# Kernel tuning notes

Measured on AMD Instinct MI355X. Metric: run time of the kernel, lower is better.

## Reference

```python
import jax, jax.numpy as jnp
import numpy as np

B, S, D = 4, 2048, 1024

def setup_inputs() -> dict:
    key = jax.random.key(0)
    k0, k1, k2, k3, k4, k5 = jax.random.split(key, 6)
    scale = 1.0 / np.sqrt(D)
    return {
        "input_seq_embs": jax.random.normal(k0, (B, S, D), dtype=jnp.float32),
        "W_Q": jax.random.normal(k1, (D, D), dtype=jnp.float32) * scale,
        "W_K": jax.random.normal(k2, (D, D), dtype=jnp.float32) * scale,
        "W_V": jax.random.normal(k3, (D, D), dtype=jnp.float32) * scale,
        "W_O": jax.random.normal(k4, (D, D), dtype=jnp.float32) * scale,
        "b_O": jax.random.normal(k5, (D,), dtype=jnp.float32) * 0.01,
    }

def reference(input_seq_embs, W_Q, W_K, W_V, W_O, b_O):
    # torch nn.Linear: y = x @ W.T
    Q = jnp.einsum('bsd,ed->bse', input_seq_embs, W_Q)
    K = jnp.einsum('bsd,ed->bse', input_seq_embs, W_K)
    V = jnp.einsum('bsd,ed->bse', input_seq_embs, W_V)
    # NOTE: no 1/sqrt(d) scaling in the original module
    A = jnp.einsum('bqd,bkd->bqk', Q, K)  # [B,S,S]
    # log(tril(ones)) == 0 on/below diagonal, -inf above
    causal = jnp.tril(jnp.ones((S, S), dtype=bool))
    A = jnp.where(causal[None, :, :], A, -jnp.inf)
    A = jax.nn.softmax(A, axis=-1)
    # dropout layers are identity in eval mode
    out = jnp.einsum('bqk,bkd->bqd', A, V)
    out = jnp.einsum('bsd,ed->bse', out, W_O) + b_O
    return out
```

## Files before the change

### kernel.cpp

```cpp
#include <hip/hip_runtime.h>
#include <cstdint>

typedef _Float16 f16x8 __attribute__((ext_vector_type(8)));
typedef _Float16 f16x4 __attribute__((ext_vector_type(4)));
typedef float    f32x4 __attribute__((ext_vector_type(4)));

#define AS1 __attribute__((address_space(1)))
#define AS3 __attribute__((address_space(3)))

__device__ __forceinline__ void load16_lds(const void* g, void* l) {
  __builtin_amdgcn_global_load_lds((AS1 void*)g, (AS3 void*)l, 16, 0, 0);
}

#define GEMM_PROLOGUE(Ab, lda, Bb, ldb)                                   \
  __shared__ _Float16 lA[128 * 32];                                       \
  __shared__ _Float16 lB[128 * 32];                                       \
  int tid = threadIdx.x;                                                  \
  int r0 = tid >> 2;                                                      \
  int c0 = (tid & 3) * 8;                                                 \
  const _Float16* ga0 = Ab + (long long)r0 * lda + c0;                    \
  const _Float16* ga1 = Ab + (long long)(r0 + 64) * lda + c0;             \
  const _Float16* gb0 = Bb + (long long)r0 * ldb + c0;                    \
  const _Float16* gb1 = Bb + (long long)(r0 + 64) * ldb + c0;             \
  _Float16* la0 = lA + tid * 8;                                           \
  _Float16* la1 = lA + 2048 + tid * 8;                                    \
  _Float16* lb0 = lB + tid * 8;                                           \
  _Float16* lb1 = lB + 2048 + tid * 8;                                    \
  f32x4 acc[4][4] = {};                                                   \
  int lane = tid & 63;                                                    \
  int wv = tid >> 6;                                                      \
  int wm = (wv & 1) * 64, wn = (wv >> 1) * 64;                            \
  int l16 = lane & 15, quad = lane >> 4;                                  \
  const _Float16* raBase = lA + (wm + l16) * 32 + quad * 8;               \
  const _Float16* rbBase = lB + (wn + l16) * 32 + quad * 8;

#define GEMM_KLOOP(lda, ldb, KLEN, SWAP)                                  \
  for (int kb = 0; kb < (KLEN); kb += 32) {                               \
    __syncthreads();                                                      \
    load16_lds(ga0, la0);                                                 \
    load16_lds(ga1, la1);                                                 \
    load16_lds(gb0, lb0);                                                 \
    load16_lds(gb1, lb1);                                                 \
    ga0 += 32; ga1 += 32; gb0 += 32; gb1 += 32;                           \
    __syncthreads();                                                      \
    f16x8 af[4], bfr[4];                                                  \
    _Pragma("unroll")                                                     \
    for (int i = 0; i < 4; i++) af[i] = *(const f16x8*)(raBase + i * 512);\
    _Pragma("unroll")                                                     \
    for (int j = 0; j < 4; j++) bfr[j] = *(const f16x8*)(rbBase + j * 512);\
    _Pragma("unroll")                                                     \
    for (int i = 0; i < 4; i++)                                           \
      _Pragma("unroll")                                                   \
      for (int j = 0; j < 4; j++)                                         \
        acc[i][j] = (SWAP)                                                \
          ? __builtin_amdgcn_mfma_f32_16x16x32_f16(bfr[j], af[i], acc[i][j], 0, 0, 0) \
          : __builtin_amdgcn_mfma_f32_16x16x32_f16(af[i], bfr[j], acc[i][j], 0, 0, 0);\
  }

__global__ __launch_bounds__(256) void cvt_all(
    const float* __restrict__ x, const float* __restrict__ wq,
    const float* __restrict__ wk, const float* __restrict__ wv,
    const float* __restrict__ wo,
    _Float16* __restrict__ xh, _Float16* __restrict__ wcat,
    _Float16* __restrict__ woh) {
  long long g = (long long)blockIdx.x * 256 + threadIdx.x;
  const float* in; _Float16* out; long long idx;
  if (g < 2097152)      { in = x;  out = xh;             idx = g; }
  else if (g < 2359296) { in = wq; out = wcat;           idx = g - 2097152; }
  else if (g < 2621440) { in = wk; out = wcat + 1048576; idx = g - 2359296; }
  else if (g < 2883584) { in = wv; out = wcat + 2097152; idx = g - 2621440; }
  else                  { in = wo; out = woh;            idx = g - 2883584; }
  float4 v = ((const float4*)in)[idx];
  f16x4 o;
  o[0] = (_Float16)v.x; o[1] = (_Float16)v.y; o[2] = (_Float16)v.z; o[3] = (_Float16)v.w;
  ((f16x4*)out)[idx] = o;
}

__global__ __launch_bounds__(256) void qk_gemm(
    const _Float16* __restrict__ A, const _Float16* __restrict__ B,
    _Float16* __restrict__ Qh, _Float16* __restrict__ Kh) {
  int bx = blockIdx.x, by = blockIdx.y;
  const _Float16* Ab = A + (long long)by * 128 * 1024;
  const _Float16* Bb = B + (long long)bx * 128 * 1024;
  GEMM_PROLOGUE(Ab, 1024, Bb, 1024)
  GEMM_KLOOP(1024, 1024, 1024, true)

  _Float16* C = (bx < 8) ? Qh : Kh;
  int m0 = by * 128 + wm + l16;
  int n0 = (bx & 7) * 128 + wn + quad * 4;
  #pragma unroll
  for (int i = 0; i < 4; i++)
    #pragma unroll
    for (int j = 0; j < 4; j++) {
      f16x4 pk;
      #pragma unroll
      for (int r = 0; r < 4; r++) pk[r] = (_Float16)acc[i][j][r];
      *(f16x4*)(C + (long long)(m0 + i * 16) * 1024 + (n0 + j * 16)) = pk;
    }
}

__global__ __launch_bounds__(256) void v_gemm(
    const _Float16* __restrict__ A, const _Float16* __restrict__ B,
    _Float16* __restrict__ Vt) {
  int bx = blockIdx.x, by = blockIdx.y;
  const _Float16* Ab = A + (long long)by * 128 * 1024;
  const _Float16* Bb = B + (long long)bx * 128 * 1024;
  GEMM_PROLOGUE(Ab, 1024, Bb, 1024)
  GEMM_KLOOP(1024, 1024, 1024, false)

  int m0 = by * 128 + wm + quad * 4;
  int d0 = bx * 128 + wn + l16;
  #pragma unroll
  for (int i = 0; i < 4; i++) {
    long long mm = m0 + i * 16;
    long long b = mm >> 11;
    long long s = mm & 2047;
    #pragma unroll
    for (int j = 0; j < 4; j++) {
      f16x4 pk;
      #pragma unroll
      for (int r = 0; r < 4; r++) pk[r] = (_Float16)acc[i][j][r];
      *(f16x4*)(Vt + (b << 21) + (long long)(d0 + j * 16) * 2048 + s) = pk;
    }
  }
}

__global__ __launch_bounds__(256) void scores_gemm(
    const _Float16* __restrict__ Qh, const _Float16* __restrict__ Kh,
    _Float16* __restrict__ S, float2* __restrict__ stats) {
  int bx = blockIdx.x, by = blockIdx.y, bz = blockIdx.z;
  if (bx > by) return;
  const _Float16* Ab = Qh + (long long)bz * 2097152 + (long long)by * 128 * 1024;
  const _Float16* Bb = Kh + (long long)bz * 2097152 + (long long)bx * 128 * 1024;
  __shared__ float redM[128];
  __shared__ float redL[128];
  GEMM_PROLOGUE(Ab, 1024, Bb, 1024)
  GEMM_KLOOP(1024, 1024, 1024, true)

  bool diag = (bx == by);
  int rloc = wm + l16;
  int cloc = wn + quad * 4;

  float mloc[4];
  #pragma unroll
  for (int i = 0; i < 4; i++) {
    float mx = -3.0e38f;
    #pragma unroll
    for (int j = 0; j < 4; j++)
      #pragma unroll
      for (int r = 0; r < 4; r++) {
        bool ok = !diag || (cloc + j * 16 + r <= rloc + i * 16);
        mx = ok ? fmaxf(mx, acc[i][j][r]) : mx;
      }
    mx = fmaxf(mx, __shfl_xor(mx, 16));
    mx = fmaxf(mx, __shfl_xor(mx, 32));
    mloc[i] = mx;
  }
  __syncthreads();
  if (wn && quad == 0) {
    #pragma unroll
    for (int i = 0; i < 4; i++) redM[rloc + i * 16] = mloc[i];
  }
  __syncthreads();
  if (!wn) {
    #pragma unroll
    for (int i = 0; i < 4; i++) mloc[i] = fmaxf(mloc[i], redM[rloc + i * 16]);
  }
  __syncthreads();
  if (!wn && quad == 0) {
    #pragma unroll
    for (int i = 0; i < 4; i++) redM[rloc + i * 16] = mloc[i];
  }
  __syncthreads();
  float mfin[4];
  #pragma unroll
  for (int i = 0; i < 4; i++) mfin[i] = redM[rloc + i * 16];

  float lloc[4];
  #pragma unroll
  for (int i = 0; i < 4; i++) {
    float sum = 0.f;
    #pragma unroll
    for (int j = 0; j < 4; j++)
      #pragma unroll
      for (int r = 0; r < 4; r++) {
        bool ok = !diag || (cloc + j * 16 + r <= rloc + i * 16);
        float e = __expf(acc[i][j][r] - mfin[i]);
        sum += ok ? e : 0.f;
      }
    sum += __shfl_xor(sum, 16);
    sum += __shfl_xor(sum, 32);
    lloc[i] = sum;
  }
  if (wn && quad == 0) {
    #pragma unroll
    for (int i = 0; i < 4; i++) redL[rloc + i * 16] = lloc[i];
  }
  __syncthreads();
  if (!wn && quad == 0) {
    #pragma unroll
    for (int i = 0; i < 4; i++) {
      int rl = rloc + i * 16;
      float lt = lloc[i] + redL[rl];
      stats[((long long)bz * 2048 + by * 128 + rl) * 16 + bx] =
          make_float2(mfin[i], lt);
    }
  }

  _Float16* Sb = S + (long long)bz * 4194304;
  int gm = by * 128 + rloc;
  int gn = bx * 128 + cloc;
  #pragma unroll
  for (int i = 0; i < 4; i++)
    #pragma unroll
    for (int j = 0; j < 4; j++) {
      f16x4 u;
      #pragma unroll
      for (int r = 0; r < 4; r++) u[r] = (_Float16)(acc[i][j][r] - mfin[i]);
      *(f16x4*)(Sb + (long long)(gm + i * 16) * 2048 + (gn + j * 16)) = u;
    }
}

__global__ __launch_bounds__(256) void normalize_p(_Float16* __restrict__ S,
                                                   const float2* __restrict__ stats) {
  int g = blockIdx.x;
  int bz = g >> 11, row = g & 2047;
  int nt = (row >> 7) + 1;
  _Float16* srow = S + ((long long)bz * 2048 + row) * 2048;
  const float2* st = stats + ((long long)bz * 2048 + row) * 16;
  __shared__ float sh_invl;
  __shared__ float shd[16];
  int t = threadIdx.x;
  if (t < 16) {
    float2 p = (t < nt) ? st[t] : make_float2(-3.0e38f, 0.f);
    float m = p.x;
    #pragma unroll
    for (int d = 1; d < 16; d <<= 1) m = fmaxf(m, __shfl_xor(m, d));
    float term = p.y * __expf(p.x - m);
    #pragma unroll
    for (int d = 1; d < 16; d <<= 1) term += __shfl_xor(term, d);
    shd[t] = p.x - m;
    if (t == 0) sh_invl = 1.0f / term;
  }
  __syncthreads();
  float invl = sh_invl;
  int Lp = nt << 7;
  for (int c = t; (c << 3) < Lp; c += 256) {
    float dt = shd[c >> 4];
    f16x8 v = ((f16x8*)srow)[c];
    f16x8 o;
    int col0 = c << 3;
    #pragma unroll
    for (int e = 0; e < 8; e++) {
      float u = (float)v[e];
      float pe = __expf(u + dt) * invl;
      o[e] = (col0 + e <= row) ? (_Float16)pe : (_Float16)0.f;
    }
    ((f16x8*)srow)[c] = o;
  }
}

__global__ __launch_bounds__(256) void pv_splitk(
    const _Float16* __restrict__ P,
    const _Float16* __restrict__ Vt,
    float* __restrict__ P0, float* __restrict__ P1,
    _Float16* __restrict__ Oh) {
  int bx = blockIdx.x, cy = blockIdx.y, bz = blockIdx.z;
  int by, c;
  if (cy < 8) { by = cy; c = 0; }
  else { int q = cy - 8; by = 8 + (q >> 1); c = q & 1; }
  int kmax = (by + 1) * 128;
  int k0 = c * 1024;
  int klen = min(kmax, k0 + 1024) - k0;

  const _Float16* Ab = P + (long long)bz * 4194304LL + (long long)by * 128 * 2048 + k0;
  const _Float16* Bb = Vt + (long long)bz * 2097152LL + (long long)bx * 128 * 2048 + k0;
  GEMM_PROLOGUE(Ab, 2048, Bb, 2048)
  GEMM_KLOOP(2048, 2048, klen, true)

  int m0 = by * 128 + wm + l16;
  int n0 = bx * 128 + wn + quad * 4;

  if (c == 0 && by < 8) {
    _Float16* C = Oh + (long long)bz * 2097152LL;
    #pragma unroll
    for (int i = 0; i < 4; i++)
      #pragma unroll
      for (int j = 0; j < 4; j++) {
        f16x4 pk;
        #pragma unroll
        for (int r = 0; r < 4; r++) pk[r] = (_Float16)acc[i][j][r];
        *(f16x4*)(C + (long long)(m0 + i * 16) * 1024 + (n0 + j * 16)) = pk;
      }
  } else if (c == 0) {
    float* C = P0 + (long long)bz * 2097152LL;
    #pragma unroll
    for (int i = 0; i < 4; i++)
      #pragma unroll
      for (int j = 0; j < 4; j++)
        *(f32x4*)(C + (long long)(m0 + i * 16) * 1024 + (n0 + j * 16)) = acc[i][j];
  } else {
    float* C = P1 + (long long)bz * 1048576LL;
    int mr = m0 - 1024;
    #pragma unroll
    for (int i = 0; i < 4; i++)
      #pragma unroll
      for (int j = 0; j < 4; j++)
        *(f32x4*)(C + (long long)(mr + i * 16) * 1024 + (n0 + j * 16)) = acc[i][j];
  }
}

__global__ __launch_bounds__(256) void pv_reduce(const float* __restrict__ P0,
                                                 const float* __restrict__ P1,
                                                 _Float16* __restrict__ Oh) {
  int i = blockIdx.x * 256 + threadIdx.x;
  if (i >= 1048576) return;
  int f4 = i;
  int bz = f4 >> 18;
  int loc = f4 & 262143;
  long long p0i = (long long)bz * 524288 + 262144 + loc;
  float4 v = ((const float4*)P0)[p0i];
  float4 w = ((const float4*)P1)[f4];
  v.x += w.x; v.y += w.y; v.z += w.z; v.w += w.w;
  f16x4 o;
  o[0] = (_Float16)v.x; o[1] = (_Float16)v.y; o[2] = (_Float16)v.z; o[3] = (_Float16)v.w;
  ((f16x4*)Oh)[p0i] = o;
}

__global__ __launch_bounds__(256) void oproj_gemm(
    const _Float16* __restrict__ A, const _Float16* __restrict__ B,
    float* __restrict__ C, const float* __restrict__ bias) {
  int bx = blockIdx.x, by = blockIdx.y;
  const _Float16* Ab = A + (long long)by * 128 * 1024;
  const _Float16* Bb = B + (long long)bx * 128 * 1024;
  GEMM_PROLOGUE(Ab, 1024, Bb, 1024)
  GEMM_KLOOP(1024, 1024, 1024, true)

  int m0 = by * 128 + wm + l16;
  int n0 = bx * 128 + wn + quad * 4;
  #pragma unroll
  for (int j = 0; j < 4; j++) {
    float4 b4 = *(const float4*)(bias + n0 + j * 16);
    #pragma unroll
    for (int i = 0; i < 4; i++) {
      f32x4 v = acc[i][j];
      v[0] += b4.x; v[1] += b4.y; v[2] += b4.z; v[3] += b4.w;
      *(f32x4*)(C + (long long)(m0 + i * 16) * 1024 + (n0 + j * 16)) = v;
    }
  }
}


extern "C" void kernel_launch(void* const* d_in, const int* in_sizes, int n_in,
                              void* d_out, int out_size, void* d_ws, size_t ws_size,
                              hipStream_t stream) {
  const float* x  = (const float*)d_in[0];
  const float* Wq = (const float*)d_in[1];
  const float* Wk = (const float*)d_in[2];
  const float* Wv = (const float*)d_in[3];
  const float* Wo = (const float*)d_in[4];
  const float* bO = (const float*)d_in[5];

  char* ws = (char*)d_ws;
  _Float16* xh   = (_Float16*)(ws + 0);
  _Float16* Wcat = (_Float16*)(ws + 16777216);
  _Float16* Woh  = (_Float16*)(ws + 23068672);
  _Float16* Qh   = (_Float16*)(ws + 25165824);
  _Float16* Kh   = (_Float16*)(ws + 41943040);
  _Float16* Vt   = (_Float16*)(ws + 58720256);
  _Float16* Oh   = (_Float16*)(ws + 75497472);
  _Float16* Sb   = (_Float16*)(ws + 92274688);
  float2*   stats= (float2*)  (ws + 125829120);
  float*    P0   = (float*)   (ws + 25165824);
  float*    P1   = (float*)   (ws + 0);

  dim3 blk(256);

  cvt_all<<<12288, blk, 0, stream>>>(x, Wq, Wk, Wv, Wo, xh, Wcat, Woh);

  qk_gemm<<<dim3(16, 64, 1), blk, 0, stream>>>(xh, Wcat, Qh, Kh);
  v_gemm<<<dim3(8, 64, 1), blk, 0, stream>>>(xh, Wcat + 2097152, Vt);

  scores_gemm<<<dim3(16, 16, 4), blk, 0, stream>>>(Qh, Kh, Sb, stats);

  normalize_p<<<8192, blk, 0, stream>>>(Sb, stats);

  pv_splitk<<<dim3(8, 24, 4), blk, 0, stream>>>(Sb, Vt, P0, P1, Oh);
  pv_reduce<<<4096, blk, 0, stream>>>(P0, P1, Oh);

  oproj_gemm<<<dim3(8, 64, 1), blk, 0, stream>>>(Oh, Woh, (float*)d_out, bO);
}
```

Baseline: 324.2 us.

## Merge QKV projection kernels and compact causal scores grid with 64-row tiles

```diff
diff --git a/kernel.cpp b/kernel.cpp
--- a/kernel.cpp
+++ b/kernel.cpp
@@ -76,51 +76,44 @@
   ((f16x4*)out)[idx] = o;
 }
 
-__global__ __launch_bounds__(256) void qk_gemm(
+__global__ __launch_bounds__(256) void qkv_gemm(
     const _Float16* __restrict__ A, const _Float16* __restrict__ B,
-    _Float16* __restrict__ Qh, _Float16* __restrict__ Kh) {
+    _Float16* __restrict__ Qh, _Float16* __restrict__ Kh, _Float16* __restrict__ Vt) {
   int bx = blockIdx.x, by = blockIdx.y;
   const _Float16* Ab = A + (long long)by * 128 * 1024;
   const _Float16* Bb = B + (long long)bx * 128 * 1024;
   GEMM_PROLOGUE(Ab, 1024, Bb, 1024)
-  GEMM_KLOOP(1024, 1024, 1024, true)
-
-  _Float16* C = (bx < 8) ? Qh : Kh;
-  int m0 = by * 128 + wm + l16;
-  int n0 = (bx & 7) * 128 + wn + quad * 4;
-  #pragma unroll
-  for (int i = 0; i < 4; i++)
-    #pragma unroll
-    for (int j = 0; j < 4; j++) {
-      f16x4 pk;
-      #pragma unroll
-      for (int r = 0; r < 4; r++) pk[r] = (_Float16)acc[i][j][r];
-      *(f16x4*)(C + (long long)(m0 + i * 16) * 1024 + (n0 + j * 16)) = pk;
-    }
-}
-
-__global__ __launch_bounds__(256) void v_gemm(
-    const _Float16* __restrict__ A, const _Float16* __restrict__ B,
-    _Float16* __restrict__ Vt) {
-  int bx = blockIdx.x, by = blockIdx.y;
-  const _Float16* Ab = A + (long long)by * 128 * 1024;
-  const _Float16* Bb = B + (long long)bx * 128 * 1024;
-  GEMM_PROLOGUE(Ab, 1024, Bb, 1024)
-  GEMM_KLOOP(1024, 1024, 1024, false)
-
-  int m0 = by * 128 + wm + quad * 4;
-  int d0 = bx * 128 + wn + l16;
-  #pragma unroll
-  for (int i = 0; i < 4; i++) {
-    long long mm = m0 + i * 16;
-    long long b = mm >> 11;
-    long long s = mm & 2047;
-    #pragma unroll
-    for (int j = 0; j < 4; j++) {
-      f16x4 pk;
-      #pragma unroll
-      for (int r = 0; r < 4; r++) pk[r] = (_Float16)acc[i][j][r];
-      *(f16x4*)(Vt + (b << 21) + (long long)(d0 + j * 16) * 2048 + s) = pk;
+
+  if (bx < 16) {
+    GEMM_KLOOP(1024, 1024, 1024, true)
+    _Float16* C = (bx < 8) ? Qh : Kh;
+    int m0 = by * 128 + wm + l16;
+    int n0 = (bx & 7) * 128 + wn + quad * 4;
+    #pragma unroll
+    for (int i = 0; i < 4; i++)
+      #pragma unroll
+      for (int j = 0; j < 4; j++) {
+        f16x4 pk;
+        #pragma unroll
+        for (int r = 0; r < 4; r++) pk[r] = (_Float16)acc[i][j][r];
+        *(f16x4*)(C + (long long)(m0 + i * 16) * 1024 + (n0 + j * 16)) = pk;
+      }
+  } else {
+    GEMM_KLOOP(1024, 1024, 1024, false)
+    int m0 = by * 128 + wm + quad * 4;
+    int d0 = (bx - 16) * 128 + wn + l16;
+    #pragma unroll
+    for (int i = 0; i < 4; i++) {
+      long long mm = m0 + i * 16;
+      long long b = mm >> 11;
+      long long s = mm & 2047;
+      #pragma unroll
+      for (int j = 0; j < 4; j++) {
+        f16x4 pk;
+        #pragma unroll
+        for (int r = 0; r < 4; r++) pk[r] = (_Float16)acc[i][j][r];
+        *(f16x4*)(Vt + (b << 21) + (long long)(d0 + j * 16) * 2048 + s) = pk;
+      }
     }
   }
 }
@@ -128,63 +121,101 @@
 __global__ __launch_bounds__(256) void scores_gemm(
     const _Float16* __restrict__ Qh, const _Float16* __restrict__ Kh,
     _Float16* __restrict__ S, float2* __restrict__ stats) {
-  int bx = blockIdx.x, by = blockIdx.y, bz = blockIdx.z;
-  if (bx > by) return;
-  const _Float16* Ab = Qh + (long long)bz * 2097152 + (long long)by * 128 * 1024;
-  const _Float16* Bb = Kh + (long long)bz * 2097152 + (long long)bx * 128 * 1024;
-  __shared__ float redM[128];
-  __shared__ float redL[128];
-  GEMM_PROLOGUE(Ab, 1024, Bb, 1024)
-  GEMM_KLOOP(1024, 1024, 1024, true)
-
-  bool diag = (bx == by);
-  int rloc = wm + l16;
-  int cloc = wn + quad * 4;
+  int t = blockIdx.x, bz = blockIdx.y;
+  int g = (int)((__builtin_sqrtf(4.0f * t + 1.0f) - 1.0f) * 0.5f);
+  while ((g + 1) * (g + 2) <= t) g++;
+  while (g * (g + 1) > t) g--;
+  int rem = t - g * (g + 1);
+  int by = 2 * g + (rem > g ? 1 : 0);
+  int bxt = (rem > g) ? rem - (g + 1) : rem;
+  bool diag = (bxt == g);
+
+  const _Float16* Ab = Qh + (long long)bz * 2097152 + (long long)by * 64 * 1024;
+  const _Float16* Bb = Kh + (long long)bz * 2097152 + (long long)bxt * 128 * 1024;
+
+  __shared__ _Float16 lA[64 * 32];
+  __shared__ _Float16 lB[128 * 32];
+  __shared__ float redM[4][64];
+  __shared__ float redL[4][64];
+
+  int tid = threadIdx.x;
+  int r0 = tid >> 2;
+  int c0 = (tid & 3) * 8;
+  const _Float16* ga0 = Ab + (long long)r0 * 1024 + c0;
+  const _Float16* gb0 = Bb + (long long)r0 * 1024 + c0;
+  const _Float16* gb1 = Bb + (long long)(r0 + 64) * 1024 + c0;
+  _Float16* la0 = lA + tid * 8;
+  _Float16* lb0 = lB + tid * 8;
+  _Float16* lb1 = lB + 2048 + tid * 8;
+
+  f32x4 acc[4][2] = {};
+  int lane = tid & 63;
+  int wv = tid >> 6;
+  int wn = wv * 32;
+  int l16 = lane & 15, quad = lane >> 4;
+  const _Float16* raBase = lA + l16 * 32 + quad * 8;
+  const _Float16* rbBase = lB + (wn + l16) * 32 + quad * 8;
+
+  for (int kb = 0; kb < 1024; kb += 32) {
+    __syncthreads();
+    load16_lds(ga0, la0);
+    load16_lds(gb0, lb0);
+    load16_lds(gb1, lb1);
+    ga0 += 32; gb0 += 32; gb1 += 32;
+    __syncthreads();
+    f16x8 af[4], bfr[2];
+    #pragma unroll
+    for (int i = 0; i < 4; i++) af[i] = *(const f16x8*)(raBase + i * 512);
+    #pragma unroll
+    for (int j = 0; j < 2; j++) bfr[j] = *(const f16x8*)(rbBase + j * 512);
+    #pragma unroll
+    for (int i = 0; i < 4; i++)
+      #pragma unroll
+      for (int j = 0; j < 2; j++)
+        acc[i][j] = __builtin_amdgcn_mfma_f32_16x16x32_f16(bfr[j], af[i], acc[i][j], 0, 0, 0);
+  }
+
+  int rowBase = by * 64;
+  int colBase = bxt * 128;
 
   float mloc[4];
   #pragma unroll
   for (int i = 0; i < 4; i++) {
+    int grow = rowBase + 16 * i + l16;
     float mx = -3.0e38f;
     #pragma unroll
-    for (int j = 0; j < 4; j++)
+    for (int j = 0; j < 2; j++)
       #pragma unroll
       for (int r = 0; r < 4; r++) {
-        bool ok = !diag || (cloc + j * 16 + r <= rloc + i * 16);
+        bool ok = !diag || (colBase + wn + 16 * j + quad * 4 + r <= grow);
         mx = ok ? fmaxf(mx, acc[i][j][r]) : mx;
       }
     mx = fmaxf(mx, __shfl_xor(mx, 16));
     mx = fmaxf(mx, __shfl_xor(mx, 32));
     mloc[i] = mx;
   }
-  __syncthreads();
-  if (wn && quad == 0) {
-    #pragma unroll
-    for (int i = 0; i < 4; i++) redM[rloc + i * 16] = mloc[i];
-  }
-  __syncthreads();
-  if (!wn) {
-    #pragma unroll
-    for (int i = 0; i < 4; i++) mloc[i] = fmaxf(mloc[i], redM[rloc + i * 16]);
-  }
-  __syncthreads();
-  if (!wn && quad == 0) {
-    #pragma unroll
-    for (int i = 0; i < 4; i++) redM[rloc + i * 16] = mloc[i];
+  if (quad == 0) {
+    #pragma unroll
+    for (int i = 0; i < 4; i++) redM[wv][16 * i + l16] = mloc[i];
   }
   __syncthreads();
   float mfin[4];
   #pragma unroll
-  for (int i = 0; i < 4; i++) mfin[i] = redM[rloc + i * 16];
+  for (int i = 0; i < 4; i++) {
+    int rl = 16 * i + l16;
+    mfin[i] = fmaxf(fmaxf(redM[0][rl], redM[1][rl]), fmaxf(redM[2][rl], redM[3][rl]));
+  }
 
   float lloc[4];
   #pragma unroll
   for (int i = 0; i < 4; i++) {
+    int grow = rowBase + 16 * i + l16;
     float sum = 0.f;
     #pragma unroll
-    for (int j = 0; j < 4; j++)
+    for (int j = 0; j < 2; j++)
       #pragma unroll
       for (int r = 0; r < 4; r++) {
-        bool ok = !diag || (cloc + j * 16 + r <= rloc + i * 16);
+        bool ok = !diag || (colBase + wn + 16 * j + quad * 4 + r <= grow);
         float e = __expf(acc[i][j][r] - mfin[i]);
         sum += ok ? e : 0.f;
       }
@@ -192,33 +223,33 @@
     sum += __shfl_xor(sum, 32);
     lloc[i] = sum;
   }
-  if (wn && quad == 0) {
-    #pragma unroll
-    for (int i = 0; i < 4; i++) redL[rloc + i * 16] = lloc[i];
+  if (quad == 0) {
+    #pragma unroll
+    for (int i = 0; i < 4; i++) redL[wv][16 * i + l16] = lloc[i];
   }
   __syncthreads();
-  if (!wn && quad == 0) {
+  if (wv == 0 && quad == 0) {
     #pragma unroll
     for (int i = 0; i < 4; i++) {
-      int rl = rloc + i * 16;
-      float lt = lloc[i] + redL[rl];
-      stats[((long long)bz * 2048 + by * 128 + rl) * 16 + bx] =
+      int rl = 16 * i + l16;
+      float lt = redL[0][rl] + redL[1][rl] + redL[2][rl] + redL[3][rl];
+      stats[((long long)bz * 2048 + rowBase + rl) * 16 + bxt] =
           make_float2(mfin[i], lt);
     }
   }
 
   _Float16* Sb = S + (long long)bz * 4194304;
-  int gm = by * 128 + rloc;
-  int gn = bx * 128 + cloc;
   #pragma unroll
-  for (int i = 0; i < 4; i++)
-    #pragma unroll
-    for (int j = 0; j < 4; j++) {
+  for (int i = 0; i < 4; i++) {
+    long long grow = rowBase + 16 * i + l16;
+    #pragma unroll
+    for (int j = 0; j < 2; j++) {
       f16x4 u;
       #pragma unroll
       for (int r = 0; r < 4; r++) u[r] = (_Float16)(acc[i][j][r] - mfin[i]);
-      *(f16x4*)(Sb + (long long)(gm + i * 16) * 2048 + (gn + j * 16)) = u;
+      *(f16x4*)(Sb + grow * 2048 + (colBase + wn + 16 * j + quad * 4)) = u;
     }
+  }
 }
 
 __global__ __launch_bounds__(256) void normalize_p(_Float16* __restrict__ S,
@@ -378,10 +409,9 @@
 
   cvt_all<<<12288, blk, 0, stream>>>(x, Wq, Wk, Wv, Wo, xh, Wcat, Woh);
 
-  qk_gemm<<<dim3(16, 64, 1), blk, 0, stream>>>(xh, Wcat, Qh, Kh);
-  v_gemm<<<dim3(8, 64, 1), blk, 0, stream>>>(xh, Wcat + 2097152, Vt);
-
-  scores_gemm<<<dim3(16, 16, 4), blk, 0, stream>>>(Qh, Kh, Sb, stats);
+  qkv_gemm<<<dim3(24, 64, 1), blk, 0, stream>>>(xh, Wcat, Qh, Kh, Vt);
+
+  scores_gemm<<<dim3(272, 4, 1), blk, 0, stream>>>(Qh, Kh, Sb, stats);
 
   normalize_p<<<8192, blk, 0, stream>>>(Sb, stats);
 
```

Result: faster. 301.1 us (-7.1%).
